# Performance work log

Hardware: AMD Instinct MI355X
Metric: run time of the kernel (lower is better)

The kernel has to match this reference:

```python
import jax, jax.numpy as jnp
import numpy as np

B, L, D = 32, 512, 128          # batch, seq_len, d_model (= num graph nodes N)
E, HS, DTR, U = 64, 64, 4, 32   # d_proj_E, d_proj_H (state), dt_rank, d_proj_U
R, K, DE, NH = 3, 3, 10, 4      # mamba layers, cheb order, d_e, heads
EPS = 1e-5


def _ln(x, g, b):
    m = jnp.mean(x, -1, keepdims=True)
    v = jnp.mean((x - m) ** 2, -1, keepdims=True)
    return (x - m) / jnp.sqrt(v + EPS) * g + b


def _mamba(x, in_w, conv_w, conv_b, xproj_w, dt_w, dt_b, Alog, Dp, out_w):
    b, l, _ = x.shape
    xz = x @ in_w                                  # (b,l,2E)
    xp, res = xz[..., :E], xz[..., E:]
    xc = jnp.transpose(xp, (0, 2, 1))              # (b,E,l)
    # causal depthwise conv: torch pads both sides by d_conv-1 then slices [:l]
    xc = jax.lax.conv_general_dilated(
        xc, conv_w, (1,), [(conv_w.shape[-1] - 1, 0)],
        dimension_numbers=('NCH', 'OIH', 'NCH'), feature_group_count=E)
    xc = xc + conv_b[None, :, None]
    xp = jax.nn.silu(jnp.transpose(xc, (0, 2, 1)))  # (b,l,E)
    xdbl = xp @ xproj_w                             # (b,l,DTR+2*HS)
    delta = jax.nn.softplus(xdbl[..., :DTR] @ dt_w + dt_b)        # (b,l,E)
    Bm = xdbl[..., DTR:DTR + HS]                                   # (b,l,HS)
    Cm = xdbl[..., DTR + HS:]                                      # (b,l,HS)
    A = -jnp.exp(Alog)                                             # (E,HS)
    dA = jnp.exp(delta[..., None] * A)                             # (b,l,E,HS)
    dBu = delta[..., None] * Bm[:, :, None, :] * xp[..., None]     # (b,l,E,HS)

    def step(s, t):
        dA_t, dBu_t, C_t = t
        s = dA_t * s + dBu_t
        return s, jnp.einsum('bdn,bn->bd', s, C_t)

    _, ys = jax.lax.scan(step, jnp.zeros((b, E, HS), x.dtype),
                         (jnp.swapaxes(dA, 0, 1), jnp.swapaxes(dBu, 0, 1),
                          jnp.swapaxes(Cm, 0, 1)))
    y = jnp.swapaxes(ys, 0, 1) + xp * Dp
    y = y * jax.nn.sigmoid(res)
    return y @ out_w


def _forward(x, mb_in_w, mb_conv_w, mb_conv_b, mb_xproj_w, mb_dt_w, mb_dt_b,
             mb_Alog, mb_D, mb_out_w, ln1_g, ln1_b, ln2_g, ln2_b,
             ffn_w1, ffn_b1, ffn_w2, ffn_b2,
             psi_emb, psi, W_q, W_k, attn_alpha, F_w, f_b, head_mix,
             head_w, head_b):
    # ---- bidirectional Mamba stack ----
    for i in range(R):
        f, bk = 2 * i, 2 * i + 1
        Y1 = _mamba(x, mb_in_w[f], mb_conv_w[f], mb_conv_b[f], mb_xproj_w[f],
                    mb_dt_w[f], mb_dt_b[f], mb_Alog[f], mb_D[f], mb_out_w[f])
        Y2 = jnp.flip(_mamba(jnp.flip(x, 1), mb_in_w[bk], mb_conv_w[bk],
                             mb_conv_b[bk], mb_xproj_w[bk], mb_dt_w[bk],
                             mb_dt_b[bk], mb_Alog[bk], mb_D[bk], mb_out_w[bk]), 1)
        Y3 = _ln(x + Y1 + Y2, ln1_g[i], ln1_b[i])
        Yp = jax.nn.relu(Y3 @ ffn_w1[i] + ffn_b1[i]) @ ffn_w2[i] + ffn_b2[i]
        x = _ln(Yp + Y3, ln2_g[i], ln2_b[i])
    h = jnp.transpose(x, (0, 2, 1))                # (B, N=D, L)
    # ---- MAGAC (deterministic single MC sample, eval, no edge drop) ----
    diff = psi_emb[:, None, :] - psi_emb[None, :, :]
    A_g = jax.nn.softmax(jnp.exp(-psi * jnp.sum(diff * diff, -1)), axis=1)
    Q = jnp.einsum('nd,dhm->nhm', psi_emb, W_q)
    Kt = jnp.einsum('nd,dhm->nhm', psi_emb, W_k)
    attn = jax.nn.softmax(jnp.einsum('nhd,mhd->hnm', Q, Kt)
                          / jnp.sqrt(jnp.asarray(DE, x.dtype)), axis=-1)
    alpha = jax.nn.sigmoid(attn_alpha)
    A_effs = alpha * A_g[None] + (1.0 - alpha) * attn   # (H,N,N)
    mix = jax.nn.softmax(head_mix)
    I = jnp.eye(D, dtype=x.dtype)
    out = jnp.zeros((x.shape[0], D), x.dtype)
    for hh in range(NH):
        A = A_effs[hh]
        sup = [I, A]
        for _ in range(2, K + 1):
            sup.append(2.0 * A @ sup[-1] - sup[-2])
        S = jnp.stack(sup, 0)                             # (K+1,N,N)
        Wf = jnp.einsum('nd,dkl->nkl', psi_emb, F_w[hh])  # (N,K+1,L)
        bf = psi_emb @ f_b[hh]                            # (N,)
        out_h = jnp.einsum('knm,bml,nkl->bn', S, h, Wf) + bf
        out = out + mix[hh] * out_h
    log_var = jnp.zeros_like(out)
    pred = out @ head_w + head_b                          # (B,1)
    return pred, log_var


def setup_inputs() -> dict:
    key = jax.random.key(0)
    ks = iter(jax.random.split(key, 40))
    nrm = lambda shp, s=0.05: (jax.random.normal(next(ks), shp, jnp.float32) * s)
    M = 2 * R
    base_Alog = jnp.log(jnp.arange(1, HS + 1, dtype=jnp.float32))
    inp = {
        'x': jax.random.normal(next(ks), (B, L, D), jnp.float32),
        'mb_in_w': nrm((M, D, 2 * E)),
        'mb_conv_w': nrm((M, E, 1, 3), 0.2),
        'mb_conv_b': jnp.zeros((M, E), jnp.float32),
        'mb_xproj_w': nrm((M, E, DTR + 2 * HS)),
        'mb_dt_w': nrm((M, DTR, E), 0.2),
        'mb_dt_b': jnp.zeros((M, E), jnp.float32),
        'mb_Alog': jnp.tile(base_Alog[None, None, :], (M, E, 1)),
        'mb_D': jnp.ones((M, E), jnp.float32),
        'mb_out_w': nrm((M, E, D)),
        'ln1_g': jnp.ones((R, D), jnp.float32),
        'ln1_b': jnp.zeros((R, D), jnp.float32),
        'ln2_g': jnp.ones((R, D), jnp.float32),
        'ln2_b': jnp.zeros((R, D), jnp.float32),
        'ffn_w1': nrm((R, D, U)),
        'ffn_b1': jnp.zeros((R, U), jnp.float32),
        'ffn_w2': nrm((R, U, D)),
        'ffn_b2': jnp.zeros((R, D), jnp.float32),
        'psi_emb': jax.random.normal(next(ks), (D, DE), jnp.float32),
        'psi': jnp.asarray(1.0, jnp.float32),
        'W_q': jax.random.normal(next(ks), (DE, NH, DE), jnp.float32),
        'W_k': jax.random.normal(next(ks), (DE, NH, DE), jnp.float32),
        'attn_alpha': jnp.asarray(0.5, jnp.float32),
        'F_w': nrm((NH, DE, K + 1, L), 0.05),
        'f_b': nrm((NH, DE), 1.0),
        'head_mix': jnp.ones((NH,), jnp.float32),
        'head_w': nrm((D, 1)),
        'head_b': jnp.zeros((1,), jnp.float32),
    }
    return inp


def reference(x, mb_in_w, mb_conv_w, mb_conv_b, mb_xproj_w, mb_dt_w, mb_dt_b,
              mb_Alog, mb_D, mb_out_w, ln1_g, ln1_b, ln2_g, ln2_b,
              ffn_w1, ffn_b1, ffn_w2, ffn_b2,
              psi_emb, psi, W_q, W_k, attn_alpha, F_w, f_b, head_mix,
              head_w, head_b):
    return _forward(x, mb_in_w, mb_conv_w, mb_conv_b, mb_xproj_w, mb_dt_w,
                    mb_dt_b, mb_Alog, mb_D, mb_out_w, ln1_g, ln1_b, ln2_g,
                    ln2_b, ffn_w1, ffn_b1, ffn_w2, ffn_b2, psi_emb, psi,
                    W_q, W_k, attn_alpha, F_w, f_b, head_mix, head_w, head_b)
```

## Files before the change

kernel.cpp:

```cpp
#include <hip/hip_runtime.h>
#include <hip/hip_bf16.h>


#define B_ 32
#define L_ 512
#define D_ 128
#define E_ 64
#define HS_ 64

#define OFF_X     0u
#define OFF_XZF   2097152u
#define OFF_XZB   4194304u
#define OFF_XPF   6291456u
#define OFF_XPB   7340032u
#define OFF_PKF   8388608u
#define OFF_PKB   10485760u
#define OFF_XBCF  12582912u
#define OFF_WFT   13631488u
#define OFF_XBCB  14680064u
#define OFF_STT   15728640u
#define OFF_AEFF  15990784u
#define OFF_YSF   16777216u
#define OFF_YSB   17825792u
#define OFF_VB    8388608u
#define OFF_PART  12582912u
#define OFF_RED1  16777216u

__device__ __forceinline__ float sigf(float x) { return 1.f / (1.f + __expf(-x)); }
__device__ __forceinline__ unsigned int bf16r(float x) {
    unsigned int u = __float_as_uint(x);
    return (u + 0x7fffu + ((u >> 16) & 1u)) >> 16;
}

__device__ void role_wf(int bx0, int tid, const float* __restrict__ psi,
                        const float* __restrict__ F_w, float* __restrict__ WfT)
{
    const int idx = bx0 * 256 + tid;
    const int n = idx & 127, l = (idx >> 7) & 511, k = (idx >> 16) & 3, h = idx >> 18;
    float acc = 0.f;
#pragma unroll
    for (int d = 0; d < 10; ++d)
        acc = fmaf(psi[n * 10 + d], F_w[((h * 10 + d) * 4 + k) * 512 + l], acc);
    WfT[idx] = acc;
}

__device__ void role_qkaeff(int bx0, int tid, const float* __restrict__ psi,
                            const float* __restrict__ psis, const float* __restrict__ W_q,
                            const float* __restrict__ W_k, const float* __restrict__ attn_a,
                            float* __restrict__ Aeff, float* __restrict__ StT,
                            float* sQ2 , float* red2 )
{
    const int half = tid >> 7, mcol = tid & 127;
    const int unit = bx0 * 2 + half;
    const int h = unit >> 7, n = unit & 127;
    float Kreg[10];
#pragma unroll
    for (int d = 0; d < 10; ++d) Kreg[d] = 0.f;
#pragma unroll
    for (int d0 = 0; d0 < 10; ++d0) {
        const float pv = psi[mcol * 10 + d0];
#pragma unroll
        for (int d = 0; d < 10; ++d) Kreg[d] = fmaf(pv, W_k[(d0 * 4 + h) * 10 + d], Kreg[d]);
    }
    if (mcol < 10) {
        float qd = 0.f;
        for (int d0 = 0; d0 < 10; ++d0)
            qd = fmaf(psi[n * 10 + d0], W_q[(d0 * 4 + h) * 10 + mcol], qd);
        sQ2[half * 16 + mcol] = qd;
    }
    __syncthreads();
    float d2 = 0.f;
#pragma unroll
    for (int d = 0; d < 10; ++d) { const float df = psi[n * 10 + d] - psi[mcol * 10 + d]; d2 = fmaf(df, df, d2); }
    const float gv = __expf(-psis[0] * d2);
    float qv = 0.f;
#pragma unroll
    for (int d = 0; d < 10; ++d) qv = fmaf(sQ2[half * 16 + d], Kreg[d], qv);
    qv *= 0.3162277660168379332f;
    float* rd = red2 + half * 128;
    float r;
    rd[mcol] = gv; __syncthreads();
    for (int s = 64; s >= 1; s >>= 1) { if (mcol < s) rd[mcol] = fmaxf(rd[mcol], rd[mcol + s]); __syncthreads(); }
    r = rd[0]; __syncthreads();
    const float eg = __expf(gv - r);
    rd[mcol] = eg; __syncthreads();
    for (int s = 64; s >= 1; s >>= 1) { if (mcol < s) rd[mcol] += rd[mcol + s]; __syncthreads(); }
    const float gsum = rd[0]; __syncthreads();
    rd[mcol] = qv; __syncthreads();
    for (int s = 64; s >= 1; s >>= 1) { if (mcol < s) rd[mcol] = fmaxf(rd[mcol], rd[mcol + s]); __syncthreads(); }
    r = rd[0]; __syncthreads();
    const float eq = __expf(qv - r);
    rd[mcol] = eq; __syncthreads();
    for (int s = 64; s >= 1; s >>= 1) { if (mcol < s) rd[mcol] += rd[mcol + s]; __syncthreads(); }
    const float qsum = rd[0];
    const float al = sigf(attn_a[0]);
    const float aeff = al * (eg / gsum) + (1.f - al) * (eq / qsum);
    Aeff[h * 16384 + n * 128 + mcol] = aeff;
    StT[((h * 4 + 1) * 128 + mcol) * 128 + n] = aeff;
    StT[((h * 4 + 0) * 128 + mcol) * 128 + n] = (mcol == n) ? 1.f : 0.f;
}

__device__ void role_cheb(int bx0, int tid, const float* __restrict__ Aeff,
                          float* __restrict__ StT, int kk)
{
    const int h = bx0 >> 6;
    const int m0 = ((bx0 & 63) << 1) + (tid >> 7);
    const int n = tid & 127;
    const float* Ar = Aeff + h * 16384 + n * 128;
    const float* Sp = StT + ((h * 4 + kk - 1) * 128 + m0) * 128;
    float acc = 0.f;
#pragma unroll 8
    for (int p = 0; p < 128; ++p) acc = fmaf(Ar[p], Sp[p], acc);
    const float s2 = StT[((h * 4 + kk - 2) * 128 + m0) * 128 + n];
    StT[((h * 4 + kk) * 128 + m0) * 128 + n] = 2.f * acc - s2;
}

__device__ void role_v4(int bx0, int tid, const float* __restrict__ StT,
                        const float* __restrict__ WfT, const float* __restrict__ hmix,
                        unsigned int* __restrict__ Vb)
{
    const float m0 = hmix[0], m1 = hmix[1], m2 = hmix[2], m3 = hmix[3];
    const float mxx = fmaxf(fmaxf(m0, m1), fmaxf(m2, m3));
    const float e0 = __expf(m0 - mxx), e1 = __expf(m1 - mxx), e2 = __expf(m2 - mxx), e3 = __expf(m3 - mxx);
    const float inv = 1.f / (e0 + e1 + e2 + e3);
    const float mixv[4] = {e0 * inv, e1 * inv, e2 * inv, e3 * inv};
    const int lt = bx0 & 63, mm = bx0 >> 6;
    const int n4 = tid & 31, mh = tid >> 5;
    const int m = mm * 8 + mh;
    const int l0 = lt * 8, n0 = n4 * 4;
    float4 sv[16];
#pragma unroll
    for (int h = 0; h < 4; ++h) {
        const float mx = mixv[h];
#pragma unroll
        for (int k = 0; k < 4; ++k) {
            const float4 v = *(const float4*)&StT[(size_t)((h * 4 + k) * 128 + m) * 128 + n0];
            sv[h * 4 + k] = float4{v.x * mx, v.y * mx, v.z * mx, v.w * mx};
        }
    }
#pragma unroll
    for (int j = 0; j < 8; ++j) {
        const int l = l0 + j;
        float4 acc = {0.f, 0.f, 0.f, 0.f};
#pragma unroll
        for (int hk = 0; hk < 16; ++hk) {
            const float4 w = *(const float4*)&WfT[(size_t)(hk * 512 + l) * 128 + n0];
            acc.x = fmaf(sv[hk].x, w.x, acc.x);
            acc.y = fmaf(sv[hk].y, w.y, acc.y);
            acc.z = fmaf(sv[hk].z, w.z, acc.z);
            acc.w = fmaf(sv[hk].w, w.w, acc.w);
        }
        const uint2 p = uint2{(bf16r(acc.y) << 16) | bf16r(acc.x),
                              (bf16r(acc.w) << 16) | bf16r(acc.z)};
        *(uint2*)&Vb[(size_t)(l * 128 + m) * 64 + (n0 >> 1)] = p;
    }
}

__global__ __launch_bounds__(256) void gemm_in2_kernel(
    const float* __restrict__ X, const float* __restrict__ WF, const float* __restrict__ WB,
    float* __restrict__ xzF, float* __restrict__ xzB)
{
    __shared__ float sxT[128][36];
    __shared__ float sw[2][16][128];
    const int tid = threadIdx.x;
    const int r0 = blockIdx.x * 32;
    for (int q = tid; q < 1024; q += 256) {
        const int r = q >> 5, k4 = q & 31;
        const float4 v = *(const float4*)&X[(size_t)(r0 + r) * 128 + k4 * 4];
        sxT[k4 * 4 + 0][r] = v.x; sxT[k4 * 4 + 1][r] = v.y;
        sxT[k4 * 4 + 2][r] = v.z; sxT[k4 * 4 + 3][r] = v.w;
    }
    const int wv = tid >> 6, lane = tid & 63;
    const int d = wv >> 1, ch = wv & 1;
    const int r4 = lane >> 4, c16 = lane & 15;
    float4 acc[8];
#pragma unroll
    for (int j = 0; j < 8; ++j) acc[j] = float4{0.f, 0.f, 0.f, 0.f};
    for (int ko = 0; ko < 128; ko += 16) {
        __syncthreads();
        for (int q = tid; q < 1024; q += 256) {
            const int dd = q >> 9, kk = (q >> 5) & 15, c4 = q & 31;
            *(float4*)&sw[dd][kk][c4 * 4] =
                *(const float4*)&((dd ? WB : WF)[(ko + kk) * 128 + c4 * 4]);
        }
        __syncthreads();
#pragma unroll
        for (int kk = 0; kk < 16; ++kk) {
            const float4 w4 = *(const float4*)&sw[d][kk][ch * 64 + c16 * 4];
            const float4 xa = *(const float4*)&sxT[ko + kk][r4 * 8];
            const float4 xb = *(const float4*)&sxT[ko + kk][r4 * 8 + 4];
            const float xs[8] = {xa.x, xa.y, xa.z, xa.w, xb.x, xb.y, xb.z, xb.w};
#pragma unroll
            for (int j = 0; j < 8; ++j) {
                acc[j].x = fmaf(xs[j], w4.x, acc[j].x);
                acc[j].y = fmaf(xs[j], w4.y, acc[j].y);
                acc[j].z = fmaf(xs[j], w4.z, acc[j].z);
                acc[j].w = fmaf(xs[j], w4.w, acc[j].w);
            }
        }
    }
    float* xz = d ? xzB : xzF;
#pragma unroll
    for (int j = 0; j < 8; ++j) {
        *(float4*)&xz[(r0 + r4 * 8 + j) * 128 + ch * 64 + c16 * 4] = acc[j];
    }
}

__global__ __launch_bounds__(256) void prep4_kernel(
    const float* __restrict__ xzF_, const float* __restrict__ xzB_,
    const float* __restrict__ conv_w, const float* __restrict__ conv_b,
    const float* __restrict__ xproj_w, const float* __restrict__ dt_w,
    const float* __restrict__ dt_b, int layer,
    float* __restrict__ xpF_, float* __restrict__ xpB_,
    unsigned int* __restrict__ xbcF_, unsigned int* __restrict__ xbcB_,
    float* __restrict__ pkF_, float* __restrict__ pkB_,
    const float* __restrict__ psi, const float* __restrict__ F_w, float* __restrict__ WfT,
    const float* __restrict__ Aeff, float* __restrict__ StT)
{
    __shared__ float sW[8448];
    __shared__ float sxp4[4][64][4];
    __shared__ float sdl4[4][4][4];
    const int tid = threadIdx.x, wv = tid >> 6, lane = tid & 63;
    if (blockIdx.x >= 2048) {
        const int bx0 = blockIdx.x - 2048;
        if (layer == 0) role_wf(bx0, tid, psi, F_w, WfT);
        else            role_cheb(bx0, tid, Aeff, StT, 3);
        return;
    }
    const int dir = (int)(blockIdx.x >= 1024);
    const int r0 = (blockIdx.x & 1023) * 16;
    const int b = r0 >> 9;
    const int m = layer * 2 + dir;
    const float* Wg = xproj_w + m * 8448;
    for (int q = tid; q < 2112; q += 256) ((float4*)sW)[q] = ((const float4*)Wg)[q];
    const float* xz = dir ? xzB_ : xzF_;
    float* xp  = dir ? xpB_  : xpF_;
    unsigned int* xbc = dir ? xbcB_ : xbcF_;
    float* pkx = dir ? pkB_  : pkF_;
    const float* cw = conv_w + m * 192 + lane * 3;
    const float cw0 = cw[0], cw1 = cw[1], cw2 = cw[2];
    const float cb  = conv_b[m * 64 + lane];
    const float dtb = dt_b[m * 64 + lane];
    const float* dwp = dt_w + m * 256;
    const float dw0 = dwp[lane], dw1 = dwp[64 + lane], dw2 = dwp[128 + lane], dw3 = dwp[192 + lane];
    float uu[4];
#pragma unroll
    for (int it = 0; it < 4; ++it) {
        const int row = r0 + wv * 4 + it;
        const int l = row & 511;
        const int l1 = dir ? l + 1 : l - 1;
        const int l2 = dir ? l + 2 : l - 2;
        float acc = cb;
        const float x0 = xz[(size_t)row * 128 + lane];
        const float x1 = (l1 >= 0 && l1 < 512) ? xz[(size_t)(b * 512 + l1) * 128 + lane] : 0.f;
        const float x2 = (l2 >= 0 && l2 < 512) ? xz[(size_t)(b * 512 + l2) * 128 + lane] : 0.f;
        acc += cw0 * x2 + cw1 * x1 + cw2 * x0;
        const float u = acc * sigf(acc);
        xp[row * 64 + lane] = u;
        uu[it] = u;
    }
    *(float4*)&sxp4[wv][lane][0] = float4{uu[0], uu[1], uu[2], uu[3]};
    __syncthreads();
    const int jdt = lane & 3;
    float aB[4] = {0.f, 0.f, 0.f, 0.f};
    float aC[4] = {0.f, 0.f, 0.f, 0.f};
    float adt[4] = {0.f, 0.f, 0.f, 0.f};
#pragma unroll 4
    for (int k = 0; k < 64; ++k) {
        const float wB = sW[k * 132 + 4 + lane];
        const float wC = sW[k * 132 + 68 + lane];
        const float wd = sW[k * 132 + jdt];
        const float4 xv = *(const float4*)&sxp4[wv][k][0];
        aB[0] = fmaf(xv.x, wB, aB[0]); aC[0] = fmaf(xv.x, wC, aC[0]); adt[0] = fmaf(xv.x, wd, adt[0]);
        aB[1] = fmaf(xv.y, wB, aB[1]); aC[1] = fmaf(xv.y, wC, aC[1]); adt[1] = fmaf(xv.y, wd, adt[1]);
        aB[2] = fmaf(xv.z, wB, aB[2]); aC[2] = fmaf(xv.z, wC, aC[2]); adt[2] = fmaf(xv.z, wd, adt[2]);
        aB[3] = fmaf(xv.w, wB, aB[3]); aC[3] = fmaf(xv.w, wC, aC[3]); adt[3] = fmaf(xv.w, wd, adt[3]);
    }
#pragma unroll
    for (int it = 0; it < 4; ++it) {
        const int row = r0 + wv * 4 + it;
        xbc[row * 64 + lane] = (bf16r(aC[it]) << 16) | bf16r(aB[it]);
        if (lane < 4) sdl4[wv][it][lane] = adt[it];
    }
#pragma unroll
    for (int it = 0; it < 4; ++it) {
        const int row = r0 + wv * 4 + it;
        float dpre = fmaf(sdl4[wv][it][0], dw0, dtb);
        dpre = fmaf(sdl4[wv][it][1], dw1, dpre);
        dpre = fmaf(sdl4[wv][it][2], dw2, dpre);
        dpre = fmaf(sdl4[wv][it][3], dw3, dpre);
        const float dlt = (dpre > 20.f) ? dpre : log1pf(__expf(dpre));
        ((float2*)pkx)[row * 64 + lane] = float2{dlt, dlt * uu[it]};
    }
}

__global__ __launch_bounds__(256, 4) void scan8_kernel(
    const unsigned int* __restrict__ xbcF, const unsigned int* __restrict__ xbcB,
    const float* __restrict__ pkF, const float* __restrict__ pkB,
    const float* __restrict__ AlogF, const float* __restrict__ AlogB,
    float* __restrict__ ysF, float* __restrict__ ysB,
    const float* __restrict__ psi, const float* __restrict__ psis,
    const float* __restrict__ W_q, const float* __restrict__ W_k,
    const float* __restrict__ attn_a, float* __restrict__ Aeff, float* __restrict__ StT)
{
    __shared__ unsigned int sbc[2][1024];
    __shared__ float spk[2][4][16][2];
    __shared__ float ytile[4][16][68];
    const int tid = threadIdx.x, wv = tid >> 6, lane = tid & 63;
    const int bx = blockIdx.x;
    if (bx >= 1024) {
        role_qkaeff(bx - 1024, tid, psi, psis, W_q, W_k, attn_a, Aeff, StT,
                    (float*)&sbc[1][0], (float*)&sbc[0][0]);
        return;
    }
    const int db = bx & 63;
    const int dir = db >> 5;
    const int b   = db & 31;
    const int e0  = (bx >> 6) * 4;
    const int e   = e0 + wv;
    const unsigned int* xbc = dir ? xbcB : xbcF;
    const float* pk  = dir ? pkB  : pkF;
    const float* Aw  = dir ? AlogB : AlogF;
    float* ys = dir ? ysB : ysF;
    const float a2 = -__expf(Aw[e * 64 + lane]) * 1.4426950408889634f;
    float s = 0.f;
    float* yrow = ys + (size_t)(b * 64 + e) * 512;

    const int psl = tid & 15, pw_ = tid >> 4;

#define STG_LOAD(RS)                                                              \
    {                                                                             \
        nb = *(const uint4*)(xbc + (size_t)(RS) * 64 + tid * 4);                  \
        if (tid < 64)                                                             \
            npp = *(const float2*)(pk + (size_t)((RS) + psl) * 128 + (e0 + pw_) * 2); \
    }
#define STG_WRITE(BUF)                                                            \
    {                                                                             \
        *(uint4*)(&sbc[BUF][tid * 4]) = nb;                                       \
        if (tid < 64) *(float2*)(&spk[BUF][pw_][psl][0]) = npp;                   \
    }

#define SCAN16(REV)                                                               \
    {                                                                             \
        const unsigned int* bc = &sbc[cur][0];                                    \
        const float* pq = &spk[cur][wv][0][0];                                    \
        _Pragma("unroll")                                                         \
        for (int j = 0; j < 8; ++j) {                                             \
            const int pj = (REV) ? 7 - j : j;                                     \
            const float4 pk4 = *(const float4*)(pq + pj * 4);                     \
            const int sA = (REV) ? 15 - 2 * j : 2 * j;                            \
            const int sB = (REV) ? 14 - 2 * j : 2 * j + 1;                        \
            const float dlA = (REV) ? pk4.z : pk4.x;                              \
            const float duA = (REV) ? pk4.w : pk4.y;                              \
            const float dlB = (REV) ? pk4.x : pk4.z;                              \
            const float duB = (REV) ? pk4.y : pk4.w;                              \
            const unsigned int bA = bc[sA * 64 + lane];                           \
            const float BnA = __uint_as_float(bA << 16);                          \
            const float CnA = __uint_as_float(bA & 0xffff0000u);                  \
            s = fmaf(__builtin_amdgcn_exp2f(dlA * a2), s, duA * BnA);             \
            ytile[wv][sA][lane] = s * CnA;                                        \
            const unsigned int bB = bc[sB * 64 + lane];                           \
            const float BnB = __uint_as_float(bB << 16);                          \
            const float CnB = __uint_as_float(bB & 0xffff0000u);                  \
            s = fmaf(__builtin_amdgcn_exp2f(dlB * a2), s, duB * BnB);             \
            ytile[wv][sB][lane] = s * CnB;                                        \
        }                                                                         \
    }

    {
        uint4 nb; float2 npp;
        const int rs0 = b * 512 + (dir ? 496 : 0);
        STG_LOAD(rs0);
        STG_WRITE(0);
    }
    __syncthreads();

    int cur = 0;
    const int rr = lane & 15, sg = lane >> 4;
    for (int t = 0; t < 32; ++t) {
        uint4 nb; float2 npp;
        const bool more = (t + 1) < 32;
        if (more) {
            const int rs = b * 512 + (dir ? (496 - (t + 1) * 16) : ((t + 1) * 16));
            STG_LOAD(rs);
        }
        if (dir == 0) { SCAN16(0) } else { SCAN16(1) }
        {
            const float* yt = &ytile[wv][rr][sg * 16];
            const float4 A0 = *(const float4*)yt;
            const float4 A1 = *(const float4*)(yt + 4);
            const float4 A2 = *(const float4*)(yt + 8);
            const float4 A3 = *(const float4*)(yt + 12);
            float p = ((A0.x + A0.y) + (A0.z + A0.w)) + ((A1.x + A1.y) + (A1.z + A1.w))
                    + ((A2.x + A2.y) + (A2.z + A2.w)) + ((A3.x + A3.y) + (A3.z + A3.w));
            p += __shfl_xor(p, 16);
            p += __shfl_xor(p, 32);
            if (lane < 16) {
                const int lg = dir ? (496 + rr - t * 16) : (t * 16 + rr);
                yrow[lg] = p;
            }
        }
        if (more) STG_WRITE(cur ^ 1);
        __syncthreads();
        cur ^= 1;
    }
#undef STG_LOAD
#undef STG_WRITE
#undef SCAN16
}

__global__ __launch_bounds__(256, 4) void opfn3_kernel(
    const float* __restrict__ ysF, const float* __restrict__ ysB,
    const float* __restrict__ xpF, const float* __restrict__ xpB,
    const float* __restrict__ xzF, const float* __restrict__ xzB,
    const float* __restrict__ Dp, int layer,
    const float* __restrict__ Xc, const float* __restrict__ out_w,
    const float* __restrict__ W1, const float* __restrict__ b1,
    const float* __restrict__ W2, const float* __restrict__ b2,
    const float* __restrict__ g1, const float* __restrict__ bb1,
    const float* __restrict__ g2, const float* __restrict__ bb2,
    float* __restrict__ xout,
    const float* __restrict__ WFn, const float* __restrict__ WBn,
    float* __restrict__ xzFo, float* __restrict__ xzBo,
    const float* __restrict__ Aeff, float* __restrict__ StT,
    const float* __restrict__ WfT, const float* __restrict__ hmix,
    unsigned int* __restrict__ Vb)
{
    __shared__ float smem[9216];
    float* syy = smem;
    float* sw  = smem + 4096;
    float* sh  = smem + 8192;
    const int tid = threadIdx.x;
    if (blockIdx.x >= 512) {
        const int bx0 = blockIdx.x - 512;
        if (layer == 0) role_cheb(bx0, tid, Aeff, StT, 2);
        else            role_v4(bx0, tid, StT, WfT, hmix, Vb);
        return;
    }
    const int r0 = blockIdx.x * 32;
    const int b = r0 >> 9, l0 = r0 & 511;
    const int wv = tid >> 6, lane = tid & 63;
    const float* WFp = out_w + (layer * 2) * 8192;
    const float* WBp = out_w + (layer * 2 + 1) * 8192;

    for (int q = tid; q < 1024; q += 256) {
        const int d = q >> 9, ee = (q >> 3) & 63, rq = q & 7;
        const float* ysp = d ? ysB : ysF;
        const float4 v = *(const float4*)&ysp[(size_t)(b * 64 + ee) * 512 + l0 + rq * 4];
        const float dv = Dp[(layer * 2 + d) * 64 + ee];
        const float* xpp = d ? xpB : xpF;
        const float* xzp = d ? xzB : xzF;
        const float vv[4] = {v.x, v.y, v.z, v.w};
#pragma unroll
        for (int j = 0; j < 4; ++j) {
            const int r = rq * 4 + j;
            const int row = r0 + r;
            const float u   = xpp[(size_t)row * 64 + ee];
            const float res = xzp[(size_t)row * 128 + 64 + ee];
            syy[r * 128 + d * 64 + ee] = (vv[j] + u * dv) * sigf(res);
        }
    }
    __syncthreads();

    float acc[8][2];
#pragma unroll
    for (int r = 0; r < 8; ++r) { acc[r][0] = 0.f; acc[r][1] = 0.f; }
#define OPSTEP8(COMP, J)                                                          \
        {                                                                         \
            const float w0 = sw[(kk + (J)) * 128 + lane];                         \
            const float w1 = sw[(kk + (J)) * 128 + lane + 64];                    \
            acc[0][0] = fmaf(y40.COMP, w0, acc[0][0]); acc[0][1] = fmaf(y40.COMP, w1, acc[0][1]); \
            acc[1][0] = fmaf(y41.COMP, w0, acc[1][0]); acc[1][1] = fmaf(y41.COMP, w1, acc[1][1]); \
            acc[2][0] = fmaf(y42.COMP, w0, acc[2][0]); acc[2][1] = fmaf(y42.COMP, w1, acc[2][1]); \
            acc[3][0] = fmaf(y43.COMP, w0, acc[3][0]); acc[3][1] = fmaf(y43.COMP, w1, acc[3][1]); \
            acc[4][0] = fmaf(y44.COMP, w0, acc[4][0]); acc[4][1] = fmaf(y44.COMP, w1, acc[4][1]); \
            acc[5][0] = fmaf(y45.COMP, w0, acc[5][0]); acc[5][1] = fmaf(y45.COMP, w1, acc[5][1]); \
            acc[6][0] = fmaf(y46.COMP, w0, acc[6][0]); acc[6][1] = fmaf(y46.COMP, w1, acc[6][1]); \
            acc[7][0] = fmaf(y47.COMP, w0, acc[7][0]); acc[7][1] = fmaf(y47.COMP, w1, acc[7][1]); \
        }
#define GEMM_CHUNK8(SRC, KO)                                                      \
    _Pragma("unroll")                                                             \
    for (int kk = 0; kk < 32; kk += 4) {                                          \
        const float4 y40 = *(const float4*)&(SRC)[(wv * 8 + 0) * 128 + (KO) + kk];\
        const float4 y41 = *(const float4*)&(SRC)[(wv * 8 + 1) * 128 + (KO) + kk];\
        const float4 y42 = *(const float4*)&(SRC)[(wv * 8 + 2) * 128 + (KO) + kk];\
        const float4 y43 = *(const float4*)&(SRC)[(wv * 8 + 3) * 128 + (KO) + kk];\
        const float4 y44 = *(const float4*)&(SRC)[(wv * 8 + 4) * 128 + (KO) + kk];\
        const float4 y45 = *(const float4*)&(SRC)[(wv * 8 + 5) * 128 + (KO) + kk];\
        const float4 y46 = *(const float4*)&(SRC)[(wv * 8 + 6) * 128 + (KO) + kk];\
        const float4 y47 = *(const float4*)&(SRC)[(wv * 8 + 7) * 128 + (KO) + kk];\
        OPSTEP8(x, 0) OPSTEP8(y, 1) OPSTEP8(z, 2) OPSTEP8(w, 3)                  \
    }
    for (int koi = 0; koi < 4; ++koi) {
        if (koi) __syncthreads();
        for (int q = tid; q < 1024; q += 256) {
            const int kk = q >> 5, c4 = q & 31;
            const int kg = koi * 32 + kk;
            *(float4*)&sw[kk * 128 + c4 * 4] = (kg < 64)
                ? *(const float4*)&WFp[kg * 128 + c4 * 4]
                : *(const float4*)&WBp[(kg - 64) * 128 + c4 * 4];
        }
        __syncthreads();
        GEMM_CHUNK8(syy, koi * 32);
    }
    __syncthreads();
    for (int q = tid; q < 1024; q += 256) ((float4*)sw)[q] = ((const float4*)W1)[q];
#pragma unroll
    for (int r = 0; r < 8; ++r) {
        const int rl = wv * 8 + r;
        const int row = r0 + rl;
        float v0 = acc[r][0] + Xc[(size_t)row * 128 + lane];
        float v1 = acc[r][1] + Xc[(size_t)row * 128 + lane + 64];
        float sum = v0 + v1, sq = v0 * v0 + v1 * v1;
#pragma unroll
        for (int o = 32; o >= 1; o >>= 1) { sum += __shfl_xor(sum, o); sq += __shfl_xor(sq, o); }
        const float mean = sum * (1.f / 128.f);
        const float var = sq * (1.f / 128.f) - mean * mean;
        const float rs = rsqrtf(var + 1e-5f);
        syy[rl * 128 + lane]      = (v0 - mean) * rs * g1[lane] + bb1[lane];
        syy[rl * 128 + lane + 64] = (v1 - mean) * rs * g1[lane + 64] + bb1[lane + 64];
    }
    __syncthreads();
    {
        const int r = tid >> 3, ug = (tid & 7) * 4;
        float h0 = b1[ug], h1 = b1[ug + 1], h2 = b1[ug + 2], h3 = b1[ug + 3];
#pragma unroll 8
        for (int k = 0; k < 128; ++k) {
            const float xv = syy[r * 128 + k];
            h0 = fmaf(xv, sw[k * 32 + ug], h0);
            h1 = fmaf(xv, sw[k * 32 + ug + 1], h1);
            h2 = fmaf(xv, sw[k * 32 + ug + 2], h2);
            h3 = fmaf(xv, sw[k * 32 + ug + 3], h3);
        }
        sh[r * 32 + ug]     = fmaxf(h0, 0.f);
        sh[r * 32 + ug + 1] = fmaxf(h1, 0.f);
        sh[r * 32 + ug + 2] = fmaxf(h2, 0.f);
        sh[r * 32 + ug + 3] = fmaxf(h3, 0.f);
    }
    __syncthreads();
    for (int q = tid; q < 1024; q += 256) ((float4*)sw)[q] = ((const float4*)W2)[q];
    __syncthreads();
    float xr[8][2];
#pragma unroll
    for (int r = 0; r < 8; ++r) {
        const int rl = wv * 8 + r;
        float a0 = b2[lane], a1 = b2[lane + 64];
#pragma unroll 8
        for (int k = 0; k < 32; ++k) {
            const float hv = sh[rl * 32 + k];
            a0 = fmaf(hv, sw[k * 128 + lane], a0);
            a1 = fmaf(hv, sw[k * 128 + lane + 64], a1);
        }
        const float v0 = a0 + syy[rl * 128 + lane];
        const float v1 = a1 + syy[rl * 128 + lane + 64];
        float sum = v0 + v1, sq = v0 * v0 + v1 * v1;
#pragma unroll
        for (int o = 32; o >= 1; o >>= 1) { sum += __shfl_xor(sum, o); sq += __shfl_xor(sq, o); }
        const float mean = sum * (1.f / 128.f);
        const float var = sq * (1.f / 128.f) - mean * mean;
        const float rs = rsqrtf(var + 1e-5f);
        const int row = r0 + rl;
        const float o0 = (v0 - mean) * rs * g2[lane] + bb2[lane];
        const float o1 = (v1 - mean) * rs * g2[lane + 64] + bb2[lane + 64];
        xout[(size_t)row * 128 + lane]      = o0;
        xout[(size_t)row * 128 + lane + 64] = o1;
        xr[r][0] = o0; xr[r][1] = o1;
    }
    if (WFn == nullptr) return;
    __syncthreads();
    float* sxr = syy;
#pragma unroll
    for (int r = 0; r < 8; ++r) {
        sxr[(wv * 8 + r) * 128 + lane]      = xr[r][0];
        sxr[(wv * 8 + r) * 128 + lane + 64] = xr[r][1];
    }
    for (int c = 0; c < 8; ++c) {
        const int dd = c >> 2, ko = (c & 3) * 32;
        const float* Wn = dd ? WBn : WFn;
        for (int q = tid; q < 1024; q += 256) {
            const int kk = q >> 5, c4 = q & 31;
            *(float4*)&sw[kk * 128 + c4 * 4] = *(const float4*)&Wn[(ko + kk) * 128 + c4 * 4];
        }
        __syncthreads();
        if ((c & 3) == 0) {
#pragma unroll
            for (int r = 0; r < 8; ++r) { acc[r][0] = 0.f; acc[r][1] = 0.f; }
        }
        GEMM_CHUNK8(sxr, ko);
        if ((c & 3) == 3) {
            float* xzo = dd ? xzBo : xzFo;
#pragma unroll
            for (int r = 0; r < 8; ++r) {
                const int row = r0 + wv * 8 + r;
                xzo[(size_t)row * 128 + lane]      = acc[r][0];
                xzo[(size_t)row * 128 + lane + 64] = acc[r][1];
            }
        }
        __syncthreads();
    }
#undef OPSTEP8
#undef GEMM_CHUNK8
}

__global__ __launch_bounds__(256) void head_ctr_kernel(
    const float* __restrict__ Xf, const unsigned int* __restrict__ Vb,
    float* __restrict__ partial)
{
    __shared__ float sx[32][128];
    const int l = blockIdx.x, tid = threadIdx.x;
    const int n = tid & 127, mh = tid >> 7;
    for (int q = tid; q < 1024; q += 256) {
        const int b = q >> 5, m4 = q & 31;
        *(float4*)&sx[b][m4 * 4] = *(const float4*)&Xf[(size_t)(b * 512 + l) * 128 + m4 * 4];
    }
    __syncthreads();
    float acc[32];
#pragma unroll
    for (int b = 0; b < 32; ++b) acc[b] = 0.f;
    const unsigned int* vp = Vb + (size_t)(l * 128 + mh * 64) * 64 + (n >> 1);
    const bool hi = (n & 1);
    for (int mm = 0; mm < 64; ++mm) {
        const unsigned int u = vp[(size_t)mm * 64];
        const float v = __uint_as_float(hi ? (u & 0xffff0000u) : (u << 16));
        const int m = mh * 64 + mm;
#pragma unroll
        for (int b = 0; b < 32; ++b) acc[b] = fmaf(sx[b][m], v, acc[b]);
    }
#pragma unroll
    for (int b = 0; b < 32; ++b)
        partial[(size_t)((l * 2 + mh) * 32 + b) * 128 + n] = acc[b];
}

__global__ __launch_bounds__(128) void head_red_kernel(
    const float* __restrict__ partial, float* __restrict__ red1)
{
    const int b = blockIdx.x >> 5, cs = blockIdx.x & 31, n = threadIdx.x;
    const float* p = partial + ((size_t)(cs * 32) * 32 + b) * 128 + n;
    float s = 0.f;
#pragma unroll 8
    for (int c = 0; c < 32; ++c) s += p[(size_t)c * 4096];
    red1[(b * 32 + cs) * 128 + n] = s;
}

__global__ __launch_bounds__(128) void head_out_kernel(
    const float* __restrict__ red1, const float* __restrict__ psi,
    const float* __restrict__ f_b, const float* __restrict__ hmix,
    const float* __restrict__ head_w, const float* __restrict__ head_b, float* __restrict__ out)
{
    __shared__ float red[128];
    const int b = blockIdx.x, n = threadIdx.x;
    const float m0 = hmix[0], m1 = hmix[1], m2 = hmix[2], m3 = hmix[3];
    const float mxx = fmaxf(fmaxf(m0, m1), fmaxf(m2, m3));
    const float e0 = __expf(m0 - mxx), e1 = __expf(m1 - mxx), e2 = __expf(m2 - mxx), e3 = __expf(m3 - mxx);
    const float inv = 1.f / (e0 + e1 + e2 + e3);
    const float mixv[4] = {e0 * inv, e1 * inv, e2 * inv, e3 * inv};
    float s = 0.f;
#pragma unroll
    for (int h = 0; h < 4; ++h) {
        float t = 0.f;
#pragma unroll
        for (int d = 0; d < 10; ++d) t = fmaf(psi[n * 10 + d], f_b[h * 10 + d], t);
        s = fmaf(mixv[h], t, s);
    }
#pragma unroll 8
    for (int cs = 0; cs < 32; ++cs) s += red1[(b * 32 + cs) * 128 + n];
    red[n] = s * head_w[n];
    __syncthreads();
    for (int st = 64; st >= 1; st >>= 1) { if (n < st) red[n] += red[n + st]; __syncthreads(); }
    if (n == 0) out[b] = red[0] + head_b[0];
    out[32 + b * 128 + n] = 0.f;
}

extern "C" void kernel_launch(void* const* d_in, const int* in_sizes, int n_in,
                              void* d_out, int out_size, void* d_ws, size_t ws_size,
                              hipStream_t stream) {
    const float* x_in    = (const float*)d_in[0];
    const float* in_w    = (const float*)d_in[1];
    const float* conv_w  = (const float*)d_in[2];
    const float* conv_b  = (const float*)d_in[3];
    const float* xproj_w = (const float*)d_in[4];
    const float* dt_w    = (const float*)d_in[5];
    const float* dt_b    = (const float*)d_in[6];
    const float* Alog    = (const float*)d_in[7];
    const float* Dp      = (const float*)d_in[8];
    const float* out_w   = (const float*)d_in[9];
    const float* ln1_g   = (const float*)d_in[10];
    const float* ln1_b   = (const float*)d_in[11];
    const float* ln2_g   = (const float*)d_in[12];
    const float* ln2_b   = (const float*)d_in[13];
    const float* ffn_w1  = (const float*)d_in[14];
    const float* ffn_b1  = (const float*)d_in[15];
    const float* ffn_w2  = (const float*)d_in[16];
    const float* ffn_b2  = (const float*)d_in[17];
    const float* psi_emb = (const float*)d_in[18];
    const float* psi_s   = (const float*)d_in[19];
    const float* W_q     = (const float*)d_in[20];
    const float* W_k     = (const float*)d_in[21];
    const float* attn_a  = (const float*)d_in[22];
    const float* F_w     = (const float*)d_in[23];
    const float* f_b     = (const float*)d_in[24];
    const float* hmix    = (const float*)d_in[25];
    const float* head_w  = (const float*)d_in[26];
    const float* head_b  = (const float*)d_in[27];
    float* ws = (float*)d_ws;
    float* outp = (float*)d_out;

    gemm_in2_kernel<<<512, 256, 0, stream>>>(
        x_in, in_w, in_w + 16384, ws + OFF_XZF, ws + OFF_XZB);
    for (int i = 0; i < 3; ++i) {
        const float* xcur = (i == 0) ? x_in : (ws + OFF_X);
        const int mF = 2 * i, mB = 2 * i + 1;
        const int prep_grid = (i == 0) ? 6144 : (i == 1) ? 2304 : 2048;
        prep4_kernel<<<prep_grid, 256, 0, stream>>>(
            ws + OFF_XZF, ws + OFF_XZB, conv_w, conv_b, xproj_w, dt_w, dt_b, i,
            ws + OFF_XPF, ws + OFF_XPB,
            (unsigned int*)(ws + OFF_XBCF), (unsigned int*)(ws + OFF_XBCB),
            ws + OFF_PKF, ws + OFF_PKB,
            psi_emb, F_w, ws + OFF_WFT, ws + OFF_AEFF, ws + OFF_STT);
        const int scan_grid = (i == 0) ? 1280 : 1024;
        scan8_kernel<<<scan_grid, 256, 0, stream>>>(
            (const unsigned int*)(ws + OFF_XBCF), (const unsigned int*)(ws + OFF_XBCB),
            ws + OFF_PKF, ws + OFF_PKB,
            Alog + mF * 4096, Alog + mB * 4096, ws + OFF_YSF, ws + OFF_YSB,
            psi_emb, psi_s, W_q, W_k, attn_a, ws + OFF_AEFF, ws + OFF_STT);
        const float* WFn = (i < 2) ? (in_w + (2 * i + 2) * 16384) : nullptr;
        const float* WBn = (i < 2) ? (in_w + (2 * i + 3) * 16384) : nullptr;
        const int opfn_grid = (i == 0) ? 768 : (i == 1) ? 512 : 1536;
        opfn3_kernel<<<opfn_grid, 256, 0, stream>>>(
            ws + OFF_YSF, ws + OFF_YSB, ws + OFF_XPF, ws + OFF_XPB, ws + OFF_XZF, ws + OFF_XZB,
            Dp, i, xcur, out_w,
            ffn_w1 + i * 4096, ffn_b1 + i * 32, ffn_w2 + i * 4096, ffn_b2 + i * 128,
            ln1_g + i * 128, ln1_b + i * 128, ln2_g + i * 128, ln2_b + i * 128,
            ws + OFF_X, WFn, WBn, ws + OFF_XZF, ws + OFF_XZB,
            ws + OFF_AEFF, ws + OFF_STT,
            ws + OFF_WFT, hmix, (unsigned int*)(ws + OFF_VB));
    }
    head_ctr_kernel<<<512, 256, 0, stream>>>(
        ws + OFF_X, (const unsigned int*)(ws + OFF_VB), ws + OFF_PART);
    head_red_kernel<<<1024, 128, 0, stream>>>(ws + OFF_PART, ws + OFF_RED1);
    head_out_kernel<<<32, 128, 0, stream>>>(
        ws + OFF_RED1, psi_emb, f_b, hmix, head_w, head_b, outp);
}
```

Measured before the change: 448.6 us.

## Fuse in-projection GEMM into prep kernel, drop standalone gemm and opfn tail GEMM

Moves the x@in_w projection out of the separate first-layer GEMM kernel and out of the tail of the previous layer's opfn kernel, and into the prep kernel. Each block loads its 16 rows plus a 2-row halo of X and computes xp, which goes straight into the causal conv, and the gate half, which is written to a smaller res buffer. This removes one launch and the round trip of the full xz tensor through global memory. In exchange the halo rows are recomputed, per-block LDS use rises, and the prep kernel does more serial FMA work per block.

Result: slower. 478.9 us (+6.8%).

```diff
diff --git a/kernel.cpp b/kernel.cpp
--- a/kernel.cpp
+++ b/kernel.cpp
@@ -9,8 +9,8 @@
 #define HS_ 64
 
 #define OFF_X     0u
-#define OFF_XZF   2097152u
-#define OFF_XZB   4194304u
+#define OFF_RESF  2097152u
+#define OFF_RESB  3145728u
 #define OFF_XPF   6291456u
 #define OFF_XPB   7340032u
 #define OFF_PKF   8388608u
@@ -156,70 +156,25 @@
     }
 }
 
-__global__ __launch_bounds__(256) void gemm_in2_kernel(
-    const float* __restrict__ X, const float* __restrict__ WF, const float* __restrict__ WB,
-    float* __restrict__ xzF, float* __restrict__ xzB)
-{
-    __shared__ float sxT[128][36];
-    __shared__ float sw[2][16][128];
-    const int tid = threadIdx.x;
-    const int r0 = blockIdx.x * 32;
-    for (int q = tid; q < 1024; q += 256) {
-        const int r = q >> 5, k4 = q & 31;
-        const float4 v = *(const float4*)&X[(size_t)(r0 + r) * 128 + k4 * 4];
-        sxT[k4 * 4 + 0][r] = v.x; sxT[k4 * 4 + 1][r] = v.y;
-        sxT[k4 * 4 + 2][r] = v.z; sxT[k4 * 4 + 3][r] = v.w;
-    }
-    const int wv = tid >> 6, lane = tid & 63;
-    const int d = wv >> 1, ch = wv & 1;
-    const int r4 = lane >> 4, c16 = lane & 15;
-    float4 acc[8];
-#pragma unroll
-    for (int j = 0; j < 8; ++j) acc[j] = float4{0.f, 0.f, 0.f, 0.f};
-    for (int ko = 0; ko < 128; ko += 16) {
-        __syncthreads();
-        for (int q = tid; q < 1024; q += 256) {
-            const int dd = q >> 9, kk = (q >> 5) & 15, c4 = q & 31;
-            *(float4*)&sw[dd][kk][c4 * 4] =
-                *(const float4*)&((dd ? WB : WF)[(ko + kk) * 128 + c4 * 4]);
-        }
-        __syncthreads();
-#pragma unroll
-        for (int kk = 0; kk < 16; ++kk) {
-            const float4 w4 = *(const float4*)&sw[d][kk][ch * 64 + c16 * 4];
-            const float4 xa = *(const float4*)&sxT[ko + kk][r4 * 8];
-            const float4 xb = *(const float4*)&sxT[ko + kk][r4 * 8 + 4];
-            const float xs[8] = {xa.x, xa.y, xa.z, xa.w, xb.x, xb.y, xb.z, xb.w};
-#pragma unroll
-            for (int j = 0; j < 8; ++j) {
-                acc[j].x = fmaf(xs[j], w4.x, acc[j].x);
-                acc[j].y = fmaf(xs[j], w4.y, acc[j].y);
-                acc[j].z = fmaf(xs[j], w4.z, acc[j].z);
-                acc[j].w = fmaf(xs[j], w4.w, acc[j].w);
-            }
-        }
-    }
-    float* xz = d ? xzB : xzF;
-#pragma unroll
-    for (int j = 0; j < 8; ++j) {
-        *(float4*)&xz[(r0 + r4 * 8 + j) * 128 + ch * 64 + c16 * 4] = acc[j];
-    }
-}
-
-__global__ __launch_bounds__(256) void prep4_kernel(
-    const float* __restrict__ xzF_, const float* __restrict__ xzB_,
+__global__ __launch_bounds__(256) void prep5_kernel(
+    const float* __restrict__ Xc, const float* __restrict__ in_w,
     const float* __restrict__ conv_w, const float* __restrict__ conv_b,
     const float* __restrict__ xproj_w, const float* __restrict__ dt_w,
     const float* __restrict__ dt_b, int layer,
     float* __restrict__ xpF_, float* __restrict__ xpB_,
     unsigned int* __restrict__ xbcF_, unsigned int* __restrict__ xbcB_,
     float* __restrict__ pkF_, float* __restrict__ pkB_,
+    float* __restrict__ resF_, float* __restrict__ resB_,
     const float* __restrict__ psi, const float* __restrict__ F_w, float* __restrict__ WfT,
     const float* __restrict__ Aeff, float* __restrict__ StT)
 {
-    __shared__ float sW[8448];
-    __shared__ float sxp4[4][64][4];
-    __shared__ float sdl4[4][4][4];
+    __shared__ float smem[9536];
+    float* sx   = smem;
+    float* sWin = smem + 2560;
+    float* sxz  = smem + 6656;
+    float* sWx  = smem;
+    float* sxp4 = smem + 8448;
+    float* sdl4 = smem + 9472;
     const int tid = threadIdx.x, wv = tid >> 6, lane = tid & 63;
     if (blockIdx.x >= 2048) {
         const int bx0 = blockIdx.x - 2048;
@@ -230,36 +185,74 @@
     const int dir = (int)(blockIdx.x >= 1024);
     const int r0 = (blockIdx.x & 1023) * 16;
     const int b = r0 >> 9;
+    const int l0 = r0 & 511;
     const int m = layer * 2 + dir;
-    const float* Wg = xproj_w + m * 8448;
-    for (int q = tid; q < 2112; q += 256) ((float4*)sW)[q] = ((const float4*)Wg)[q];
-    const float* xz = dir ? xzB_ : xzF_;
     float* xp  = dir ? xpB_  : xpF_;
     unsigned int* xbc = dir ? xbcB_ : xbcF_;
     float* pkx = dir ? pkB_  : pkF_;
+    float* res = dir ? resB_ : resF_;
     const float* cw = conv_w + m * 192 + lane * 3;
     const float cw0 = cw[0], cw1 = cw[1], cw2 = cw[2];
     const float cb  = conv_b[m * 64 + lane];
     const float dtb = dt_b[m * 64 + lane];
     const float* dwp = dt_w + m * 256;
     const float dw0 = dwp[lane], dw1 = dwp[64 + lane], dw2 = dwp[128 + lane], dw3 = dwp[192 + lane];
+
+    for (int q = tid; q < 640; q += 256) {
+        const int lr = q >> 5, c4 = q & 31;
+        const int l = l0 - 2 + lr;
+        float4 v = float4{0.f, 0.f, 0.f, 0.f};
+        if (l >= 0 && l < 512) v = *(const float4*)&Xc[(size_t)(b * 512 + l) * 128 + c4 * 4];
+        *(float4*)&sx[lr * 128 + c4 * 4] = v;
+    }
+    float accx[5] = {0.f, 0.f, 0.f, 0.f, 0.f};
+    float accr[4] = {0.f, 0.f, 0.f, 0.f};
+    const float* Wg2 = in_w + m * 16384;
+    for (int kc = 0; kc < 4; ++kc) {
+        __syncthreads();
+        for (int q = tid; q < 1024; q += 256) {
+            const int kk = q >> 5, c4 = q & 31;
+            *(float4*)&sWin[kk * 128 + c4 * 4] = *(const float4*)&Wg2[(kc * 32 + kk) * 128 + c4 * 4];
+        }
+        __syncthreads();
+#pragma unroll 8
+        for (int kk = 0; kk < 32; ++kk) {
+            const float wx = sWin[kk * 128 + lane];
+            const float wr = sWin[kk * 128 + 64 + lane];
+            const int kg = kc * 32 + kk;
+            accx[0] = fmaf(sx[(5 * wv + 0) * 128 + kg], wx, accx[0]);
+            accx[1] = fmaf(sx[(5 * wv + 1) * 128 + kg], wx, accx[1]);
+            accx[2] = fmaf(sx[(5 * wv + 2) * 128 + kg], wx, accx[2]);
+            accx[3] = fmaf(sx[(5 * wv + 3) * 128 + kg], wx, accx[3]);
+            accx[4] = fmaf(sx[(5 * wv + 4) * 128 + kg], wx, accx[4]);
+            accr[0] = fmaf(sx[(2 + 4 * wv + 0) * 128 + kg], wr, accr[0]);
+            accr[1] = fmaf(sx[(2 + 4 * wv + 1) * 128 + kg], wr, accr[1]);
+            accr[2] = fmaf(sx[(2 + 4 * wv + 2) * 128 + kg], wr, accr[2]);
+            accr[3] = fmaf(sx[(2 + 4 * wv + 3) * 128 + kg], wr, accr[3]);
+        }
+    }
+#pragma unroll
+    for (int j = 0; j < 5; ++j) sxz[(5 * wv + j) * 64 + lane] = accx[j];
+#pragma unroll
+    for (int j = 0; j < 4; ++j) res[(size_t)(r0 + 4 * wv + j) * 64 + lane] = accr[j];
+    __syncthreads();
     float uu[4];
 #pragma unroll
     for (int it = 0; it < 4; ++it) {
-        const int row = r0 + wv * 4 + it;
-        const int l = row & 511;
-        const int l1 = dir ? l + 1 : l - 1;
-        const int l2 = dir ? l + 2 : l - 2;
-        float acc = cb;
-        const float x0 = xz[(size_t)row * 128 + lane];
-        const float x1 = (l1 >= 0 && l1 < 512) ? xz[(size_t)(b * 512 + l1) * 128 + lane] : 0.f;
-        const float x2 = (l2 >= 0 && l2 < 512) ? xz[(size_t)(b * 512 + l2) * 128 + lane] : 0.f;
-        acc += cw0 * x2 + cw1 * x1 + cw2 * x0;
+        const int lloc = 2 + wv * 4 + it;
+        const int o1 = dir ? 1 : -1;
+        const float x0 = sxz[lloc * 64 + lane];
+        const float x1 = sxz[(lloc + o1) * 64 + lane];
+        const float x2 = sxz[(lloc + 2 * o1) * 64 + lane];
+        float acc = cb + cw0 * x2 + cw1 * x1 + cw2 * x0;
         const float u = acc * sigf(acc);
-        xp[row * 64 + lane] = u;
+        xp[(size_t)(r0 + wv * 4 + it) * 64 + lane] = u;
         uu[it] = u;
     }
-    *(float4*)&sxp4[wv][lane][0] = float4{uu[0], uu[1], uu[2], uu[3]};
+    __syncthreads();
+    const float* Wg = xproj_w + m * 8448;
+    for (int q = tid; q < 2112; q += 256) ((float4*)sWx)[q] = ((const float4*)Wg)[q];
+    *(float4*)&sxp4[(wv * 64 + lane) * 4] = float4{uu[0], uu[1], uu[2], uu[3]};
     __syncthreads();
     const int jdt = lane & 3;
     float aB[4] = {0.f, 0.f, 0.f, 0.f};
@@ -267,10 +260,10 @@
     float adt[4] = {0.f, 0.f, 0.f, 0.f};
 #pragma unroll 4
     for (int k = 0; k < 64; ++k) {
-        const float wB = sW[k * 132 + 4 + lane];
-        const float wC = sW[k * 132 + 68 + lane];
-        const float wd = sW[k * 132 + jdt];
-        const float4 xv = *(const float4*)&sxp4[wv][k][0];
+        const float wB = sWx[k * 132 + 4 + lane];
+        const float wC = sWx[k * 132 + 68 + lane];
+        const float wd = sWx[k * 132 + jdt];
+        const float4 xv = *(const float4*)&sxp4[(wv * 64 + k) * 4];
         aB[0] = fmaf(xv.x, wB, aB[0]); aC[0] = fmaf(xv.x, wC, aC[0]); adt[0] = fmaf(xv.x, wd, adt[0]);
         aB[1] = fmaf(xv.y, wB, aB[1]); aC[1] = fmaf(xv.y, wC, aC[1]); adt[1] = fmaf(xv.y, wd, adt[1]);
         aB[2] = fmaf(xv.z, wB, aB[2]); aC[2] = fmaf(xv.z, wC, aC[2]); adt[2] = fmaf(xv.z, wd, adt[2]);
@@ -280,15 +273,15 @@
     for (int it = 0; it < 4; ++it) {
         const int row = r0 + wv * 4 + it;
         xbc[row * 64 + lane] = (bf16r(aC[it]) << 16) | bf16r(aB[it]);
-        if (lane < 4) sdl4[wv][it][lane] = adt[it];
+        if (lane < 4) sdl4[(wv * 4 + it) * 4 + lane] = adt[it];
     }
 #pragma unroll
     for (int it = 0; it < 4; ++it) {
         const int row = r0 + wv * 4 + it;
-        float dpre = fmaf(sdl4[wv][it][0], dw0, dtb);
-        dpre = fmaf(sdl4[wv][it][1], dw1, dpre);
-        dpre = fmaf(sdl4[wv][it][2], dw2, dpre);
-        dpre = fmaf(sdl4[wv][it][3], dw3, dpre);
+        float dpre = fmaf(sdl4[(wv * 4 + it) * 4 + 0], dw0, dtb);
+        dpre = fmaf(sdl4[(wv * 4 + it) * 4 + 1], dw1, dpre);
+        dpre = fmaf(sdl4[(wv * 4 + it) * 4 + 2], dw2, dpre);
+        dpre = fmaf(sdl4[(wv * 4 + it) * 4 + 3], dw3, dpre);
         const float dlt = (dpre > 20.f) ? dpre : log1pf(__expf(dpre));
         ((float2*)pkx)[row * 64 + lane] = float2{dlt, dlt * uu[it]};
     }
@@ -409,10 +402,10 @@
 #undef SCAN16
 }
 
-__global__ __launch_bounds__(256, 4) void opfn3_kernel(
+__global__ __launch_bounds__(256, 4) void opfn4_kernel(
     const float* __restrict__ ysF, const float* __restrict__ ysB,
     const float* __restrict__ xpF, const float* __restrict__ xpB,
-    const float* __restrict__ xzF, const float* __restrict__ xzB,
+    const float* __restrict__ resF, const float* __restrict__ resB,
     const float* __restrict__ Dp, int layer,
     const float* __restrict__ Xc, const float* __restrict__ out_w,
     const float* __restrict__ W1, const float* __restrict__ b1,
@@ -420,8 +413,6 @@
     const float* __restrict__ g1, const float* __restrict__ bb1,
     const float* __restrict__ g2, const float* __restrict__ bb2,
     float* __restrict__ xout,
-    const float* __restrict__ WFn, const float* __restrict__ WBn,
-    float* __restrict__ xzFo, float* __restrict__ xzBo,
     const float* __restrict__ Aeff, float* __restrict__ StT,
     const float* __restrict__ WfT, const float* __restrict__ hmix,
     unsigned int* __restrict__ Vb)
@@ -449,15 +440,15 @@
         const float4 v = *(const float4*)&ysp[(size_t)(b * 64 + ee) * 512 + l0 + rq * 4];
         const float dv = Dp[(layer * 2 + d) * 64 + ee];
         const float* xpp = d ? xpB : xpF;
-        const float* xzp = d ? xzB : xzF;
+        const float* rsp = d ? resB : resF;
         const float vv[4] = {v.x, v.y, v.z, v.w};
 #pragma unroll
         for (int j = 0; j < 4; ++j) {
             const int r = rq * 4 + j;
             const int row = r0 + r;
             const float u   = xpp[(size_t)row * 64 + ee];
-            const float res = xzp[(size_t)row * 128 + 64 + ee];
-            syy[r * 128 + d * 64 + ee] = (vv[j] + u * dv) * sigf(res);
+            const float rsv = rsp[(size_t)row * 64 + ee];
+            syy[r * 128 + d * 64 + ee] = (vv[j] + u * dv) * sigf(rsv);
         }
     }
     __syncthreads();
@@ -540,7 +531,6 @@
     __syncthreads();
     for (int q = tid; q < 1024; q += 256) ((float4*)sw)[q] = ((const float4*)W2)[q];
     __syncthreads();
-    float xr[8][2];
 #pragma unroll
     for (int r = 0; r < 8; ++r) {
         const int rl = wv * 8 + r;
@@ -560,46 +550,9 @@
         const float var = sq * (1.f / 128.f) - mean * mean;
         const float rs = rsqrtf(var + 1e-5f);
         const int row = r0 + rl;
-        const float o0 = (v0 - mean) * rs * g2[lane] + bb2[lane];
-        const float o1 = (v1 - mean) * rs * g2[lane + 64] + bb2[lane + 64];
-        xout[(size_t)row * 128 + lane]      = o0;
-        xout[(size_t)row * 128 + lane + 64] = o1;
-        xr[r][0] = o0; xr[r][1] = o1;
-    }
-    if (WFn == nullptr) return;
-    __syncthreads();
-    float* sxr = syy;
-#pragma unroll
-    for (int r = 0; r < 8; ++r) {
-        sxr[(wv * 8 + r) * 128 + lane]      = xr[r][0];
-        sxr[(wv * 8 + r) * 128 + lane + 64] = xr[r][1];
-    }
-    for (int c = 0; c < 8; ++c) {
-        const int dd = c >> 2, ko = (c & 3) * 32;
-        const float* Wn = dd ? WBn : WFn;
-        for (int q = tid; q < 1024; q += 256) {
-            const int kk = q >> 5, c4 = q & 31;
-            *(float4*)&sw[kk * 128 + c4 * 4] = *(const float4*)&Wn[(ko + kk) * 128 + c4 * 4];
-        }
-        __syncthreads();
-        if ((c & 3) == 0) {
-#pragma unroll
-            for (int r = 0; r < 8; ++r) { acc[r][0] = 0.f; acc[r][1] = 0.f; }
-        }
-        GEMM_CHUNK8(sxr, ko);
-        if ((c & 3) == 3) {
-            float* xzo = dd ? xzBo : xzFo;
-#pragma unroll
-            for (int r = 0; r < 8; ++r) {
-                const int row = r0 + wv * 8 + r;
-                xzo[(size_t)row * 128 + lane]      = acc[r][0];
-                xzo[(size_t)row * 128 + lane + 64] = acc[r][1];
-            }
-        }
-        __syncthreads();
-    }
-#undef OPSTEP8
-#undef GEMM_CHUNK8
+        xout[(size_t)row * 128 + lane]      = (v0 - mean) * rs * g2[lane] + bb2[lane];
+        xout[(size_t)row * 128 + lane + 64] = (v1 - mean) * rs * g2[lane + 64] + bb2[lane + 64];
+    }
 }
 
 __global__ __launch_bounds__(256) void head_ctr_kernel(
@@ -705,17 +658,16 @@
     float* ws = (float*)d_ws;
     float* outp = (float*)d_out;
 
-    gemm_in2_kernel<<<512, 256, 0, stream>>>(
-        x_in, in_w, in_w + 16384, ws + OFF_XZF, ws + OFF_XZB);
     for (int i = 0; i < 3; ++i) {
         const float* xcur = (i == 0) ? x_in : (ws + OFF_X);
         const int mF = 2 * i, mB = 2 * i + 1;
         const int prep_grid = (i == 0) ? 6144 : (i == 1) ? 2304 : 2048;
-        prep4_kernel<<<prep_grid, 256, 0, stream>>>(
-            ws + OFF_XZF, ws + OFF_XZB, conv_w, conv_b, xproj_w, dt_w, dt_b, i,
+        prep5_kernel<<<prep_grid, 256, 0, stream>>>(
+            xcur, in_w, conv_w, conv_b, xproj_w, dt_w, dt_b, i,
             ws + OFF_XPF, ws + OFF_XPB,
             (unsigned int*)(ws + OFF_XBCF), (unsigned int*)(ws + OFF_XBCB),
             ws + OFF_PKF, ws + OFF_PKB,
+            ws + OFF_RESF, ws + OFF_RESB,
             psi_emb, F_w, ws + OFF_WFT, ws + OFF_AEFF, ws + OFF_STT);
         const int scan_grid = (i == 0) ? 1280 : 1024;
         scan8_kernel<<<scan_grid, 256, 0, stream>>>(
@@ -723,15 +675,14 @@
             ws + OFF_PKF, ws + OFF_PKB,
             Alog + mF * 4096, Alog + mB * 4096, ws + OFF_YSF, ws + OFF_YSB,
             psi_emb, psi_s, W_q, W_k, attn_a, ws + OFF_AEFF, ws + OFF_STT);
-        const float* WFn = (i < 2) ? (in_w + (2 * i + 2) * 16384) : nullptr;
-        const float* WBn = (i < 2) ? (in_w + (2 * i + 3) * 16384) : nullptr;
         const int opfn_grid = (i == 0) ? 768 : (i == 1) ? 512 : 1536;
-        opfn3_kernel<<<opfn_grid, 256, 0, stream>>>(
-            ws + OFF_YSF, ws + OFF_YSB, ws + OFF_XPF, ws + OFF_XPB, ws + OFF_XZF, ws + OFF_XZB,
+        opfn4_kernel<<<opfn_grid, 256, 0, stream>>>(
+            ws + OFF_YSF, ws + OFF_YSB, ws + OFF_XPF, ws + OFF_XPB,
+            ws + OFF_RESF, ws + OFF_RESB,
             Dp, i, xcur, out_w,
             ffn_w1 + i * 4096, ffn_b1 + i * 32, ffn_w2 + i * 4096, ffn_b2 + i * 128,
             ln1_g + i * 128, ln1_b + i * 128, ln2_g + i * 128, ln2_b + i * 128,
-            ws + OFF_X, WFn, WBn, ws + OFF_XZF, ws + OFF_XZB,
+            ws + OFF_X,
             ws + OFF_AEFF, ws + OFF_STT,
             ws + OFF_WFT, hmix, (unsigned int*)(ws + OFF_VB));
     }
```
